# Performance work log

Hardware: AMD Instinct MI355X
Metric: run time of the kernel (lower is better)

The kernel has to match this reference:

```python
import jax, jax.numpy as jnp
import numpy as np

EPS_BN = 1e-5
EPS_NORM = 1e-12
USER_NUM, ITEM_NUM = 100000, 50000
N_NODES = USER_NUM + ITEM_NUM
N_EDGES = 2400000
OUT_DIM, HID_DIM = 64, 128
BATCH = 4096


def setup_inputs() -> dict:
    key = jax.random.key(0)
    ks = jax.random.split(key, 12)
    f32 = jnp.float32
    return {
        "user_emb": jax.random.normal(ks[0], (USER_NUM, OUT_DIM), f32) * 0.1,
        "item_emb": jax.random.normal(ks[1], (ITEM_NUM, OUT_DIM), f32) * 0.1,
        "W0": jax.random.normal(ks[2], (OUT_DIM, HID_DIM), f32) * (1.0 / np.sqrt(OUT_DIM)),
        "b0": jnp.zeros((HID_DIM,), f32),
        "g0": jnp.ones((HID_DIM,), f32),
        "beta0": jnp.zeros((HID_DIM,), f32),
        "W1": jax.random.normal(ks[3], (HID_DIM, HID_DIM), f32) * (1.0 / np.sqrt(HID_DIM)),
        "b1": jnp.zeros((HID_DIM,), f32),
        "g1": jnp.ones((HID_DIM,), f32),
        "beta1": jnp.zeros((HID_DIM,), f32),
        "W2": jax.random.normal(ks[4], (HID_DIM, OUT_DIM), f32) * (1.0 / np.sqrt(HID_DIM)),
        "b2": jnp.zeros((OUT_DIM,), f32),
        "user_id": jax.random.randint(ks[5], (BATCH,), 0, USER_NUM),
        "pos_item": jax.random.randint(ks[6], (BATCH,), 0, ITEM_NUM),
        "neg_item": jax.random.randint(ks[7], (BATCH,), 0, ITEM_NUM),
        "edge_index": jax.random.randint(ks[8], (2, N_EDGES), 0, N_NODES),
    }


def _gcn_conv(x, W, b, src, dst, dis):
    # GCNConv with self-loops and symmetric normalization:
    # out_i = sum_{j->i} d_j^{-1/2} d_i^{-1/2} (x_j W) + d_i^{-1} (x_i W) + b
    h = x @ W                                   # [N, F]
    norm = dis[src] * dis[dst]                  # [E]
    msgs = h[src] * norm[:, None]               # [E, F] (irregular gather)
    agg = jax.ops.segment_sum(msgs, dst, num_segments=x.shape[0])
    self_loop = h * (dis * dis)[:, None]        # contribution of added self-loops
    return agg + self_loop + b


def _bn_train(x, gamma, beta):
    mean = jnp.mean(x, axis=0)
    var = jnp.mean((x - mean) ** 2, axis=0)     # biased var, as torch BN uses
    return (x - mean) * jax.lax.rsqrt(var + EPS_BN) * gamma + beta


def _l2norm(x):
    n = jnp.sqrt(jnp.sum(x * x, axis=-1, keepdims=True))
    return x / jnp.maximum(n, EPS_NORM)


def reference(user_emb, item_emb, W0, b0, g0, beta0, W1, b1, g1, beta1, W2, b2,
              user_id, pos_item, neg_item, edge_index):
    N = user_emb.shape[0] + item_emb.shape[0]
    src, dst = edge_index[0], edge_index[1]
    # degree includes self loop (weight 1 per edge + 1 self loop)
    deg = 1.0 + jax.ops.segment_sum(jnp.ones_like(src, user_emb.dtype), dst, num_segments=N)
    dis = jax.lax.rsqrt(deg)

    x = jnp.concatenate([user_emb, item_emb], axis=0)          # [N, OUT_DIM]

    # layer 0: conv -> BN -> ReLU -> (dropout: eval/identity) -> L2-normalize
    x = _l2norm(jax.nn.relu(_bn_train(_gcn_conv(x, W0, b0, src, dst, dis), g0, beta0)))
    # layer 1
    x = _l2norm(jax.nn.relu(_bn_train(_gcn_conv(x, W1, b1, src, dst, dis), g1, beta1)))
    # final conv
    x = _gcn_conv(x, W2, b2, src, dst, dis)                    # [N, OUT_DIM]

    user_embeddings = x[:user_emb.shape[0]]
    item_embeddings = x[user_emb.shape[0]:]
    u = user_embeddings[user_id]
    p = item_embeddings[pos_item]
    n = item_embeddings[neg_item]
    pos_score = jnp.sum(u * p, axis=-1)
    neg_score = jnp.sum(u * n, axis=-1)
    rec_loss = -jnp.mean(jax.nn.log_sigmoid(pos_score - neg_score))
    return rec_loss, x
```

## Files before the change

kernel.cpp:

```cpp
#include <hip/hip_runtime.h>
#include <hip/hip_bf16.h>
#include <math.h>

#define USER_NUM 100000
#define ITEM_NUM 50000
#define N_NODES  150000
#define N_EDGES  2400000
#define OUT_DIM  64
#define HID_DIM  128
#define BATCH    4096
#define EPS_BN   1e-5f

typedef unsigned short ushort_t;
typedef unsigned int uint_t;

typedef __attribute__((ext_vector_type(8))) __bf16 bf16x8;
typedef __attribute__((ext_vector_type(4))) float f32x4;

__device__ __forceinline__ ushort_t f2bf(float f) {
    uint_t u = __float_as_uint(f);
    u += 0x7FFFu + ((u >> 16) & 1u);
    return (ushort_t)(u >> 16);
}
__device__ __forceinline__ float bf2f(ushort_t s) {
    return __uint_as_float((uint_t)s << 16);
}


__global__ __launch_bounds__(256) void zero_int_kernel(int* __restrict__ p, int n) {
    int i = blockIdx.x * 256 + threadIdx.x;
    if (i < n) p[i] = 0;
}

__global__ __launch_bounds__(256) void count_kernel(const int* __restrict__ dst, int* __restrict__ cnt) {
    int i = blockIdx.x * 256 + threadIdx.x;
    if (i < N_EDGES) atomicAdd(&cnt[dst[i]], 1);
}

__global__ __launch_bounds__(256) void dis_kernel(const int* __restrict__ cnt, float* __restrict__ dis) {
    int i = blockIdx.x * 256 + threadIdx.x;
    if (i < N_NODES) dis[i] = rsqrtf(1.0f + (float)cnt[i]);
}

#define SC_ELEM 1024
#define SC_NB   ((N_NODES + SC_ELEM - 1) / SC_ELEM)

__global__ __launch_bounds__(256) void scan_part_kernel(const int* __restrict__ cnt,
                                                        int* __restrict__ psum) {
    __shared__ int red[4];
    int tid = threadIdx.x;
    int base = blockIdx.x * SC_ELEM + tid * 4;
    int s = 0;
#pragma unroll
    for (int j = 0; j < 4; j++) { int i = base + j; if (i < N_NODES) s += cnt[i]; }
#pragma unroll
    for (int d = 1; d < 64; d <<= 1) s += __shfl_xor(s, d);
    if ((tid & 63) == 0) red[tid >> 6] = s;
    __syncthreads();
    if (tid == 0) psum[blockIdx.x] = red[0] + red[1] + red[2] + red[3];
}

__global__ __launch_bounds__(256) void scan_mid_kernel(int* __restrict__ psum,
                                                       int* __restrict__ off, int nb) {
    __shared__ int lds[256];
    int tid = threadIdx.x;
    int v = (tid < nb) ? psum[tid] : 0;
    lds[tid] = v;
    __syncthreads();
    for (int d = 1; d < 256; d <<= 1) {
        int t = (tid >= d) ? lds[tid - d] : 0;
        __syncthreads();
        lds[tid] += t;
        __syncthreads();
    }
    if (tid < nb) psum[tid] = lds[tid] - v;
    if (tid == 0) off[N_NODES] = lds[255];
}

__global__ __launch_bounds__(256) void scan_emit_kernel(const int* __restrict__ cnt,
                                                        const int* __restrict__ psum,
                                                        int* __restrict__ off) {
    __shared__ int lds[256];
    int tid = threadIdx.x;
    int base = blockIdx.x * SC_ELEM + tid * 4;
    int v[4]; int s = 0;
#pragma unroll
    for (int j = 0; j < 4; j++) {
        int i = base + j;
        v[j] = (i < N_NODES) ? cnt[i] : 0;
        s += v[j];
    }
    lds[tid] = s;
    __syncthreads();
    for (int d = 1; d < 256; d <<= 1) {
        int t = (tid >= d) ? lds[tid - d] : 0;
        __syncthreads();
        lds[tid] += t;
        __syncthreads();
    }
    int run = psum[blockIdx.x] + lds[tid] - s;
#pragma unroll
    for (int j = 0; j < 4; j++) {
        int i = base + j;
        if (i < N_NODES) off[i] = run;
        run += v[j];
    }
}


#define BSH   9
#define NBUCK ((N_NODES + 511) / 512)
#define P1_BLOCKS 512

__global__ __launch_bounds__(256) void bucket_part_kernel(const int* __restrict__ src,
                                                          const int* __restrict__ dst,
                                                          const int* __restrict__ off,
                                                          int* __restrict__ bcur,
                                                          uint2* __restrict__ temp) {
    __shared__ int hist[NBUCK];
    __shared__ int base[NBUCK];
    const int per = (N_EDGES + P1_BLOCKS - 1) / P1_BLOCKS;
    const int lo = blockIdx.x * per;
    int hi = lo + per; if (hi > N_EDGES) hi = N_EDGES;
    const int tid = threadIdx.x;
    for (int j = tid; j < NBUCK; j += 256) hist[j] = 0;
    __syncthreads();
    for (int i = lo + tid; i < hi; i += 256)
        atomicAdd(&hist[dst[i] >> BSH], 1);
    __syncthreads();
    for (int b = tid; b < NBUCK; b += 256) {
        int h = hist[b];
        if (h > 0) base[b] = off[b << BSH] + atomicAdd(&bcur[b], h);
    }
    __syncthreads();
    for (int i = lo + tid; i < hi; i += 256) {
        int d = dst[i];
        int p = atomicAdd(&base[d >> BSH], 1);
        temp[p] = make_uint2((uint_t)src[i], (uint_t)d);
    }
}

__global__ __launch_bounds__(256) void bucket_fine_kernel(const int* __restrict__ off,
                                                          const float* __restrict__ dis,
                                                          const uint2* __restrict__ temp,
                                                          uint2* __restrict__ csr8) {
    __shared__ int   offs[513];
    __shared__ int   cur[512];
    __shared__ float disd[512];
    const int b  = blockIdx.x;
    const int lo = b << BSH;
    int hi = lo + 512; if (hi > N_NODES) hi = N_NODES;
    const int nn = hi - lo;
    const int tid = threadIdx.x;
    for (int j = tid; j <= nn; j += 256) offs[j] = off[lo + j];
    for (int j = tid; j < nn; j += 256) { cur[j] = 0; disd[j] = dis[lo + j]; }
    __syncthreads();
    const int e0 = offs[0], e1 = offs[nn];
    for (int i = e0 + tid; i < e1; i += 256) {
        uint2 t = temp[i];
        int dl = (int)t.y - lo;
        int p = offs[dl] + atomicAdd(&cur[dl], 1);
        float wv = dis[t.x] * disd[dl];
        csr8[p] = make_uint2(t.x, __float_as_uint(wv));
    }
}


__device__ __forceinline__ bf16x8 loadA(const ushort_t* p) {
    uint4 u = *(const uint4*)p;
    return __builtin_bit_cast(bf16x8, u);
}
__device__ __forceinline__ bf16x8 loadA(const float* p) {
    float4 f0 = *(const float4*)p;
    float4 f1 = *(const float4*)(p + 4);
    uint4 u;
    u.x = (uint_t)f2bf(f0.x) | ((uint_t)f2bf(f0.y) << 16);
    u.y = (uint_t)f2bf(f0.z) | ((uint_t)f2bf(f0.w) << 16);
    u.z = (uint_t)f2bf(f1.x) | ((uint_t)f2bf(f1.y) << 16);
    u.w = (uint_t)f2bf(f1.z) | ((uint_t)f2bf(f1.w) << 16);
    return __builtin_bit_cast(bf16x8, u);
}

template<typename XT, int DIN, int DOUT>
__global__ __launch_bounds__(256) void gemm_kernel(const XT* __restrict__ xlo,
                                                   const XT* __restrict__ xhi, int split,
                                                   const float* __restrict__ W,
                                                   ushort_t* __restrict__ out, int nrows) {
    constexpr int LDW = DIN + 8;
    constexpr int NCT = DOUT / 16;
    __shared__ ushort_t wt[DOUT][LDW];

    const int tid = threadIdx.x;
    for (int idx = tid; idx < DIN * DOUT; idx += 256) {
        int k = idx / DOUT, n = idx % DOUT;
        wt[n][k] = f2bf(W[idx]);
    }
    __syncthreads();

    const int wave = tid >> 6, lane = tid & 63;
    const int lm = lane & 15, lk = lane >> 4;
    const int row0 = blockIdx.x * 128 + wave * 32;

    f32x4 acc[2][NCT];
#pragma unroll
    for (int rt = 0; rt < 2; rt++)
#pragma unroll
        for (int c = 0; c < NCT; c++) acc[rt][c] = (f32x4){0.f, 0.f, 0.f, 0.f};

    const XT* rp[2];
#pragma unroll
    for (int rt = 0; rt < 2; rt++) {
        int row = row0 + rt * 16 + lm;
        if (row > nrows - 1) row = nrows - 1;
        rp[rt] = (row < split) ? xlo + (size_t)row * DIN
                               : xhi + (size_t)(row - split) * DIN;
    }

#pragma unroll
    for (int ks = 0; ks < DIN / 32; ks++) {
        bf16x8 a0 = loadA(rp[0] + ks * 32 + lk * 8);
        bf16x8 a1 = loadA(rp[1] + ks * 32 + lk * 8);
#pragma unroll
        for (int c = 0; c < NCT; c++) {
            bf16x8 b = *(const bf16x8*)&wt[c * 16 + lm][ks * 32 + lk * 8];
            acc[0][c] = __builtin_amdgcn_mfma_f32_16x16x32_bf16(a0, b, acc[0][c], 0, 0, 0);
            acc[1][c] = __builtin_amdgcn_mfma_f32_16x16x32_bf16(a1, b, acc[1][c], 0, 0, 0);
        }
    }

#pragma unroll
    for (int rt = 0; rt < 2; rt++) {
#pragma unroll
        for (int r = 0; r < 4; r++) {
            int row = row0 + rt * 16 + lk * 4 + r;
            if (row < nrows) {
#pragma unroll
                for (int c = 0; c < NCT; c++)
                    out[(size_t)row * DOUT + c * 16 + lm] = f2bf(acc[rt][c][r]);
            }
        }
    }
}


template<int DOUT>
__global__ __launch_bounds__(256) void agg_kernel(const ushort_t* __restrict__ h,
                                                  const float* __restrict__ dis,
                                                  const int* __restrict__ off,
                                                  const uint2* __restrict__ csr8,
                                                  const float* __restrict__ bias,
                                                  float* __restrict__ out, int n) {
    int wave = threadIdx.x >> 6;
    int lane = threadIdx.x & 63;
    int node = blockIdx.x * 4 + wave;
    if (node >= n) return;
    float di  = dis[node];
    int   beg = off[node], end = off[node + 1];
    if (DOUT == 128) {
        const uint_t* hp = (const uint_t*)h;
        float ax = 0.f, ay = 0.f;
        int e = beg;
        for (; e + 4 <= end; e += 4) {
            uint2 e0 = csr8[e], e1 = csr8[e + 1], e2 = csr8[e + 2], e3 = csr8[e + 3];
            uint_t u0 = hp[(size_t)e0.x * 64 + lane];
            uint_t u1 = hp[(size_t)e1.x * 64 + lane];
            uint_t u2 = hp[(size_t)e2.x * 64 + lane];
            uint_t u3 = hp[(size_t)e3.x * 64 + lane];
            float w0 = __uint_as_float(e0.y), w1 = __uint_as_float(e1.y);
            float w2 = __uint_as_float(e2.y), w3 = __uint_as_float(e3.y);
            ax = fmaf(__uint_as_float(u0 << 16), w0, ax);
            ay = fmaf(__uint_as_float(u0 & 0xFFFF0000u), w0, ay);
            ax = fmaf(__uint_as_float(u1 << 16), w1, ax);
            ay = fmaf(__uint_as_float(u1 & 0xFFFF0000u), w1, ay);
            ax = fmaf(__uint_as_float(u2 << 16), w2, ax);
            ay = fmaf(__uint_as_float(u2 & 0xFFFF0000u), w2, ay);
            ax = fmaf(__uint_as_float(u3 << 16), w3, ax);
            ay = fmaf(__uint_as_float(u3 & 0xFFFF0000u), w3, ay);
        }
        for (; e < end; e++) {
            uint2 ev = csr8[e];
            float wv = __uint_as_float(ev.y);
            uint_t u = hp[(size_t)ev.x * 64 + lane];
            ax = fmaf(__uint_as_float(u << 16), wv, ax);
            ay = fmaf(__uint_as_float(u & 0xFFFF0000u), wv, ay);
        }
        uint_t us = hp[(size_t)node * 64 + lane];
        float2 bb = ((const float2*)bias)[lane];
        float dd = di * di;
        float2 o;
        o.x = ax + __uint_as_float(us << 16) * dd + bb.x;
        o.y = ay + __uint_as_float(us & 0xFFFF0000u) * dd + bb.y;
        ((float2*)out)[(size_t)node * 64 + lane] = o;
    } else {
        float ax = 0.f;
        int e = beg;
        for (; e + 4 <= end; e += 4) {
            uint2 e0 = csr8[e], e1 = csr8[e + 1], e2 = csr8[e + 2], e3 = csr8[e + 3];
            float h0 = bf2f(h[(size_t)e0.x * 64 + lane]);
            float h1 = bf2f(h[(size_t)e1.x * 64 + lane]);
            float h2 = bf2f(h[(size_t)e2.x * 64 + lane]);
            float h3 = bf2f(h[(size_t)e3.x * 64 + lane]);
            ax = fmaf(h0, __uint_as_float(e0.y), ax);
            ax = fmaf(h1, __uint_as_float(e1.y), ax);
            ax = fmaf(h2, __uint_as_float(e2.y), ax);
            ax = fmaf(h3, __uint_as_float(e3.y), ax);
        }
        for (; e < end; e++) {
            uint2 ev = csr8[e];
            ax = fmaf(bf2f(h[(size_t)ev.x * 64 + lane]), __uint_as_float(ev.y), ax);
        }
        float hs = bf2f(h[(size_t)node * 64 + lane]);
        out[(size_t)node * 64 + lane] = ax + hs * di * di + bias[lane];
    }
}


#define STATS_NB 512

__global__ __launch_bounds__(128) void stats1_kernel(const float* __restrict__ x,
                                                     double* __restrict__ part) {
    int col = threadIdx.x;
    double a = 0.0, b = 0.0;
    for (int row = blockIdx.x; row < N_NODES; row += STATS_NB) {
        float v = x[(size_t)row * HID_DIM + col];
        a += v;
        b += (double)v * (double)v;
    }
    part[(size_t)blockIdx.x * 256 + col]       = a;
    part[(size_t)blockIdx.x * 256 + 128 + col] = b;
}

__global__ __launch_bounds__(256) void stats2_kernel(const double* __restrict__ part,
                                                     const float* __restrict__ g,
                                                     const float* __restrict__ beta,
                                                     float* __restrict__ a_out,
                                                     float* __restrict__ b_out) {
    __shared__ double red1[4], red2[4];
    int col = blockIdx.x;
    int tid = threadIdx.x;
    double s1 = 0.0, s2 = 0.0;
    for (int p = tid; p < STATS_NB; p += 256) {
        s1 += part[(size_t)p * 256 + col];
        s2 += part[(size_t)p * 256 + 128 + col];
    }
#pragma unroll
    for (int d = 32; d >= 1; d >>= 1) {
        s1 += __shfl_xor(s1, d);
        s2 += __shfl_xor(s2, d);
    }
    int wave = tid >> 6, lane = tid & 63;
    if (lane == 0) { red1[wave] = s1; red2[wave] = s2; }
    __syncthreads();
    if (tid == 0) {
        double t1 = red1[0] + red1[1] + red1[2] + red1[3];
        double t2 = red2[0] + red2[1] + red2[2] + red2[3];
        double mean = t1 / (double)N_NODES;
        double var  = t2 / (double)N_NODES - mean * mean;
        float inv = rsqrtf((float)var + EPS_BN);
        float aa  = g[col] * inv;
        a_out[col] = aa;
        b_out[col] = beta[col] - (float)mean * aa;
    }
}


__global__ __launch_bounds__(256) void bn_relu_l2_kernel(const float* __restrict__ in,
                                                         const float* __restrict__ a,
                                                         const float* __restrict__ b,
                                                         uint_t* __restrict__ outp, int n) {
    int wave = threadIdx.x >> 6;
    int lane = threadIdx.x & 63;
    int row  = blockIdx.x * 4 + wave;
    if (row >= n) return;
    float2 v  = *(const float2*)(in + (size_t)row * 128 + lane * 2);
    float2 aa = *(const float2*)(a + lane * 2);
    float2 bb = *(const float2*)(b + lane * 2);
    float y0 = fmaxf(fmaf(v.x, aa.x, bb.x), 0.f);
    float y1 = fmaxf(fmaf(v.y, aa.y, bb.y), 0.f);
    float ss = y0 * y0 + y1 * y1;
#pragma unroll
    for (int d = 32; d >= 1; d >>= 1) ss += __shfl_xor(ss, d);
    float nn  = sqrtf(ss);
    float inv = 1.f / fmaxf(nn, 1e-12f);
    uint_t pk = (uint_t)f2bf(y0 * inv) | ((uint_t)f2bf(y1 * inv) << 16);
    outp[(size_t)row * 64 + lane] = pk;
}


__global__ void zero_float_kernel(float* p) { *p = 0.f; }

__global__ __launch_bounds__(256) void loss_kernel(const float* __restrict__ X,
                                                   const int* __restrict__ uid,
                                                   const int* __restrict__ pid,
                                                   const int* __restrict__ nid,
                                                   float* __restrict__ out0) {
    int wave = threadIdx.x >> 6;
    int lane = threadIdx.x & 63;
    int b = blockIdx.x * 4 + wave;
    if (b >= BATCH) return;
    const float* u = X + (size_t)uid[b] * OUT_DIM;
    const float* p = X + (size_t)(USER_NUM + pid[b]) * OUT_DIM;
    const float* q = X + (size_t)(USER_NUM + nid[b]) * OUT_DIM;
    float uv = u[lane];
    float ps = uv * p[lane];
    float ns = uv * q[lane];
#pragma unroll
    for (int d = 32; d >= 1; d >>= 1) {
        ps += __shfl_xor(ps, d);
        ns += __shfl_xor(ns, d);
    }
    if (lane == 0) {
        float t  = ns - ps;
        float sp = fmaxf(t, 0.f) + log1pf(expf(-fabsf(t)));
        atomicAdd(out0, sp * (1.0f / BATCH));
    }
}


extern "C" void kernel_launch(void* const* d_in, const int* in_sizes, int n_in,
                              void* d_out, int out_size, void* d_ws, size_t ws_size,
                              hipStream_t stream) {
    const float* user_emb = (const float*)d_in[0];
    const float* item_emb = (const float*)d_in[1];
    const float* W0  = (const float*)d_in[2];
    const float* b0  = (const float*)d_in[3];
    const float* g0  = (const float*)d_in[4];
    const float* be0 = (const float*)d_in[5];
    const float* W1  = (const float*)d_in[6];
    const float* b1  = (const float*)d_in[7];
    const float* g1  = (const float*)d_in[8];
    const float* be1 = (const float*)d_in[9];
    const float* W2  = (const float*)d_in[10];
    const float* b2  = (const float*)d_in[11];
    const int* user_id  = (const int*)d_in[12];
    const int* pos_item = (const int*)d_in[13];
    const int* neg_item = (const int*)d_in[14];
    const int* edge     = (const int*)d_in[15];
    const int* src = edge;
    const int* dst = edge + N_EDGES;

    char* w = (char*)d_ws;
    auto alloc = [&](size_t bytes) -> char* {
        char* r = w;
        w += (bytes + 255) / 256 * 256;
        return r;
    };
    int*      cnt  = (int*)alloc((size_t)N_NODES * 4);
    int*      off  = (int*)alloc((size_t)(N_NODES + 1) * 4);
    int*      bcur = (int*)alloc((size_t)NBUCK * 4);
    uint2*    csr8 = (uint2*)alloc((size_t)N_EDGES * 8);
    float*    dis  = (float*)alloc((size_t)N_NODES * 4);
    int*      psum = (int*)alloc((size_t)SC_NB * 4);
    double*   part = (double*)alloc((size_t)STATS_NB * 256 * 8);
    float*    bn_a = (float*)alloc(128 * 4);
    float*    bn_b = (float*)alloc(128 * 4);
    ushort_t* hbuf = (ushort_t*)alloc((size_t)N_NODES * HID_DIM * 2);
    float*    xbuf = (float*)alloc((size_t)N_NODES * HID_DIM * 4);
    ushort_t* xbf  = (ushort_t*)alloc((size_t)N_NODES * HID_DIM * 2);

    uint2* temp = (uint2*)hbuf;

    float* out = (float*)d_out;
    float* X   = out + 1;

    const int EB = (N_EDGES + 255) / 256;
    const int NB = (N_NODES + 255) / 256;
    const int AGGB = (N_NODES + 3) / 4;
    const int GB = (N_NODES + 127) / 128;

    zero_int_kernel<<<NB, 256, 0, stream>>>(cnt, N_NODES);
    count_kernel<<<EB, 256, 0, stream>>>(dst, cnt);
    dis_kernel<<<NB, 256, 0, stream>>>(cnt, dis);
    scan_part_kernel<<<SC_NB, 256, 0, stream>>>(cnt, psum);
    scan_mid_kernel<<<1, 256, 0, stream>>>(psum, off, SC_NB);
    scan_emit_kernel<<<SC_NB, 256, 0, stream>>>(cnt, psum, off);
    zero_int_kernel<<<(NBUCK + 255) / 256, 256, 0, stream>>>(bcur, NBUCK);
    bucket_part_kernel<<<P1_BLOCKS, 256, 0, stream>>>(src, dst, off, bcur, temp);
    bucket_fine_kernel<<<NBUCK, 256, 0, stream>>>(off, dis, temp, csr8);

    gemm_kernel<float, 64, 128><<<GB, 256, 0, stream>>>(
        user_emb, item_emb, USER_NUM, W0, hbuf, N_NODES);
    agg_kernel<128><<<AGGB, 256, 0, stream>>>(hbuf, dis, off, csr8, b0, xbuf, N_NODES);
    stats1_kernel<<<STATS_NB, 128, 0, stream>>>(xbuf, part);
    stats2_kernel<<<128, 256, 0, stream>>>(part, g0, be0, bn_a, bn_b);
    bn_relu_l2_kernel<<<AGGB, 256, 0, stream>>>(xbuf, bn_a, bn_b, (uint_t*)xbf, N_NODES);

    gemm_kernel<ushort_t, 128, 128><<<GB, 256, 0, stream>>>(
        xbf, xbf, N_NODES, W1, hbuf, N_NODES);
    agg_kernel<128><<<AGGB, 256, 0, stream>>>(hbuf, dis, off, csr8, b1, xbuf, N_NODES);
    stats1_kernel<<<STATS_NB, 128, 0, stream>>>(xbuf, part);
    stats2_kernel<<<128, 256, 0, stream>>>(part, g1, be1, bn_a, bn_b);
    bn_relu_l2_kernel<<<AGGB, 256, 0, stream>>>(xbuf, bn_a, bn_b, (uint_t*)xbf, N_NODES);

    gemm_kernel<ushort_t, 128, 64><<<GB, 256, 0, stream>>>(
        xbf, xbf, N_NODES, W2, hbuf, N_NODES);
    agg_kernel<64><<<AGGB, 256, 0, stream>>>(hbuf, dis, off, csr8, b2, X, N_NODES);

    zero_float_kernel<<<1, 1, 0, stream>>>(out);
    loss_kernel<<<(BATCH + 3) / 4, 256, 0, stream>>>(X, user_id, pos_item, neg_item, out);
}
```

Before: 967.5 us.

## Fuse BN statistics into persistent aggregation kernel with deeper gather unroll

Result: no change. 955.1 us (-1.3%).

```diff
diff --git a/kernel.cpp b/kernel.cpp
--- a/kernel.cpp
+++ b/kernel.cpp
@@ -13,6 +13,7 @@
 
 typedef unsigned short ushort_t;
 typedef unsigned int uint_t;
+typedef unsigned long long ull_t;
 
 typedef __attribute__((ext_vector_type(8))) __bf16 bf16x8;
 typedef __attribute__((ext_vector_type(4))) float f32x4;
@@ -236,101 +237,111 @@
             if (row < nrows) {
 #pragma unroll
                 for (int c = 0; c < NCT; c++)
-                    out[(size_t)row * DOUT + c * 16 + lm] = f2bf(acc[rt][c][r]);
+                    __builtin_nontemporal_store(f2bf(acc[rt][c][r]),
+                                                &out[(size_t)row * DOUT + c * 16 + lm]);
             }
         }
     }
 }
 
 
-template<int DOUT>
+#define AGG_BLOCKS 2048
+#define NPART (AGG_BLOCKS * 4)
+
+template<int DOUT, bool STATS>
 __global__ __launch_bounds__(256) void agg_kernel(const ushort_t* __restrict__ h,
                                                   const float* __restrict__ dis,
                                                   const int* __restrict__ off,
                                                   const uint2* __restrict__ csr8,
                                                   const float* __restrict__ bias,
-                                                  float* __restrict__ out, int n) {
-    int wave = threadIdx.x >> 6;
-    int lane = threadIdx.x & 63;
-    int node = blockIdx.x * 4 + wave;
-    if (node >= n) return;
-    float di  = dis[node];
-    int   beg = off[node], end = off[node + 1];
-    if (DOUT == 128) {
-        const uint_t* hp = (const uint_t*)h;
-        float ax = 0.f, ay = 0.f;
-        int e = beg;
-        for (; e + 4 <= end; e += 4) {
-            uint2 e0 = csr8[e], e1 = csr8[e + 1], e2 = csr8[e + 2], e3 = csr8[e + 3];
-            uint_t u0 = hp[(size_t)e0.x * 64 + lane];
-            uint_t u1 = hp[(size_t)e1.x * 64 + lane];
-            uint_t u2 = hp[(size_t)e2.x * 64 + lane];
-            uint_t u3 = hp[(size_t)e3.x * 64 + lane];
-            float w0 = __uint_as_float(e0.y), w1 = __uint_as_float(e1.y);
-            float w2 = __uint_as_float(e2.y), w3 = __uint_as_float(e3.y);
-            ax = fmaf(__uint_as_float(u0 << 16), w0, ax);
-            ay = fmaf(__uint_as_float(u0 & 0xFFFF0000u), w0, ay);
-            ax = fmaf(__uint_as_float(u1 << 16), w1, ax);
-            ay = fmaf(__uint_as_float(u1 & 0xFFFF0000u), w1, ay);
-            ax = fmaf(__uint_as_float(u2 << 16), w2, ax);
-            ay = fmaf(__uint_as_float(u2 & 0xFFFF0000u), w2, ay);
-            ax = fmaf(__uint_as_float(u3 << 16), w3, ax);
-            ay = fmaf(__uint_as_float(u3 & 0xFFFF0000u), w3, ay);
+                                                  float* __restrict__ out,
+                                                  float* __restrict__ part, int n) {
+    const int wave = threadIdx.x >> 6;
+    const int lane = threadIdx.x & 63;
+    const int gw   = blockIdx.x * 4 + wave;
+    const int NW   = AGG_BLOCKS * 4;
+
+    float s1x = 0.f, s2x = 0.f, s1y = 0.f, s2y = 0.f;
+
+    for (int node = gw; node < n; node += NW) {
+        float di  = dis[node];
+        int   beg = off[node], end = off[node + 1];
+        if (DOUT == 128) {
+            const uint_t* hp = (const uint_t*)h;
+            float ax = 0.f, ay = 0.f;
+            int e = beg;
+            for (; e + 8 <= end; e += 8) {
+                ull_t c[8];
+#pragma unroll
+                for (int j = 0; j < 8; j++)
+                    c[j] = __builtin_nontemporal_load((const ull_t*)&csr8[e + j]);
+                uint_t u[8];
+#pragma unroll
+                for (int j = 0; j < 8; j++)
+                    u[j] = hp[(size_t)(uint_t)c[j] * 64 + lane];
+#pragma unroll
+                for (int j = 0; j < 8; j++) {
+                    float wv = __uint_as_float((uint_t)(c[j] >> 32));
+                    ax = fmaf(__uint_as_float(u[j] << 16), wv, ax);
+                    ay = fmaf(__uint_as_float(u[j] & 0xFFFF0000u), wv, ay);
+                }
+            }
+            for (; e < end; e++) {
+                ull_t cv = __builtin_nontemporal_load((const ull_t*)&csr8[e]);
+                float wv = __uint_as_float((uint_t)(cv >> 32));
+                uint_t u = hp[(size_t)(uint_t)cv * 64 + lane];
+                ax = fmaf(__uint_as_float(u << 16), wv, ax);
+                ay = fmaf(__uint_as_float(u & 0xFFFF0000u), wv, ay);
+            }
+            uint_t us = hp[(size_t)node * 64 + lane];
+            float2 bb = ((const float2*)bias)[lane];
+            float dd = di * di;
+            float ox = ax + __uint_as_float(us << 16) * dd + bb.x;
+            float oy = ay + __uint_as_float(us & 0xFFFF0000u) * dd + bb.y;
+            ull_t obits = __builtin_bit_cast(ull_t, make_float2(ox, oy));
+            __builtin_nontemporal_store(obits, (ull_t*)&((float2*)out)[(size_t)node * 64 + lane]);
+            if (STATS) {
+                s1x += ox; s2x = fmaf(ox, ox, s2x);
+                s1y += oy; s2y = fmaf(oy, oy, s2y);
+            }
+        } else {
+            float ax = 0.f;
+            int e = beg;
+            for (; e + 8 <= end; e += 8) {
+                ull_t c[8];
+#pragma unroll
+                for (int j = 0; j < 8; j++)
+                    c[j] = __builtin_nontemporal_load((const ull_t*)&csr8[e + j]);
+                float hv[8];
+#pragma unroll
+                for (int j = 0; j < 8; j++)
+                    hv[j] = bf2f(h[(size_t)(uint_t)c[j] * 64 + lane]);
+#pragma unroll
+                for (int j = 0; j < 8; j++)
+                    ax = fmaf(hv[j], __uint_as_float((uint_t)(c[j] >> 32)), ax);
+            }
+            for (; e < end; e++) {
+                ull_t cv = __builtin_nontemporal_load((const ull_t*)&csr8[e]);
+                ax = fmaf(bf2f(h[(size_t)(uint_t)cv * 64 + lane]),
+                          __uint_as_float((uint_t)(cv >> 32)), ax);
+            }
+            float hs = bf2f(h[(size_t)node * 64 + lane]);
+            float ox = ax + hs * di * di + bias[lane];
+            __builtin_nontemporal_store(ox, &out[(size_t)node * 64 + lane]);
         }
-        for (; e < end; e++) {
-            uint2 ev = csr8[e];
-            float wv = __uint_as_float(ev.y);
-            uint_t u = hp[(size_t)ev.x * 64 + lane];
-            ax = fmaf(__uint_as_float(u << 16), wv, ax);
-            ay = fmaf(__uint_as_float(u & 0xFFFF0000u), wv, ay);
-        }
-        uint_t us = hp[(size_t)node * 64 + lane];
-        float2 bb = ((const float2*)bias)[lane];
-        float dd = di * di;
-        float2 o;
-        o.x = ax + __uint_as_float(us << 16) * dd + bb.x;
-        o.y = ay + __uint_as_float(us & 0xFFFF0000u) * dd + bb.y;
-        ((float2*)out)[(size_t)node * 64 + lane] = o;
-    } else {
-        float ax = 0.f;
-        int e = beg;
-        for (; e + 4 <= end; e += 4) {
-            uint2 e0 = csr8[e], e1 = csr8[e + 1], e2 = csr8[e + 2], e3 = csr8[e + 3];
-            float h0 = bf2f(h[(size_t)e0.x * 64 + lane]);
-            float h1 = bf2f(h[(size_t)e1.x * 64 + lane]);
-            float h2 = bf2f(h[(size_t)e2.x * 64 + lane]);
-            float h3 = bf2f(h[(size_t)e3.x * 64 + lane]);
-            ax = fmaf(h0, __uint_as_float(e0.y), ax);
-            ax = fmaf(h1, __uint_as_float(e1.y), ax);
-            ax = fmaf(h2, __uint_as_float(e2.y), ax);
-            ax = fmaf(h3, __uint_as_float(e3.y), ax);
-        }
-        for (; e < end; e++) {
-            uint2 ev = csr8[e];
-            ax = fmaf(bf2f(h[(size_t)ev.x * 64 + lane]), __uint_as_float(ev.y), ax);
-        }
-        float hs = bf2f(h[(size_t)node * 64 + lane]);
-        out[(size_t)node * 64 + lane] = ax + hs * di * di + bias[lane];
-    }
-}
-
-
-#define STATS_NB 512
-
-__global__ __launch_bounds__(128) void stats1_kernel(const float* __restrict__ x,
-                                                     double* __restrict__ part) {
-    int col = threadIdx.x;
-    double a = 0.0, b = 0.0;
-    for (int row = blockIdx.x; row < N_NODES; row += STATS_NB) {
-        float v = x[(size_t)row * HID_DIM + col];
-        a += v;
-        b += (double)v * (double)v;
-    }
-    part[(size_t)blockIdx.x * 256 + col]       = a;
-    part[(size_t)blockIdx.x * 256 + 128 + col] = b;
-}
-
-__global__ __launch_bounds__(256) void stats2_kernel(const double* __restrict__ part,
+    }
+
+    if (STATS) {
+        float* pp = part + (size_t)gw * 256;
+        pp[lane * 2]           = s1x;
+        pp[lane * 2 + 1]       = s1y;
+        pp[128 + lane * 2]     = s2x;
+        pp[128 + lane * 2 + 1] = s2y;
+    }
+}
+
+
+__global__ __launch_bounds__(256) void stats2_kernel(const float* __restrict__ part,
                                                      const float* __restrict__ g,
                                                      const float* __restrict__ beta,
                                                      float* __restrict__ a_out,
@@ -339,9 +350,9 @@
     int col = blockIdx.x;
     int tid = threadIdx.x;
     double s1 = 0.0, s2 = 0.0;
-    for (int p = tid; p < STATS_NB; p += 256) {
-        s1 += part[(size_t)p * 256 + col];
-        s2 += part[(size_t)p * 256 + 128 + col];
+    for (int p = tid; p < NPART; p += 256) {
+        s1 += (double)part[(size_t)p * 256 + col];
+        s2 += (double)part[(size_t)p * 256 + 128 + col];
     }
 #pragma unroll
     for (int d = 32; d >= 1; d >>= 1) {
@@ -451,7 +462,7 @@
     uint2*    csr8 = (uint2*)alloc((size_t)N_EDGES * 8);
     float*    dis  = (float*)alloc((size_t)N_NODES * 4);
     int*      psum = (int*)alloc((size_t)SC_NB * 4);
-    double*   part = (double*)alloc((size_t)STATS_NB * 256 * 8);
+    float*    part = (float*)alloc((size_t)NPART * 256 * 4);
     float*    bn_a = (float*)alloc(128 * 4);
     float*    bn_b = (float*)alloc(128 * 4);
     ushort_t* hbuf = (ushort_t*)alloc((size_t)N_NODES * HID_DIM * 2);
@@ -465,7 +476,7 @@
 
     const int EB = (N_EDGES + 255) / 256;
     const int NB = (N_NODES + 255) / 256;
-    const int AGGB = (N_NODES + 3) / 4;
+    const int BNB = (N_NODES + 3) / 4;
     const int GB = (N_NODES + 127) / 128;
 
     zero_int_kernel<<<NB, 256, 0, stream>>>(cnt, N_NODES);
@@ -480,21 +491,22 @@
 
     gemm_kernel<float, 64, 128><<<GB, 256, 0, stream>>>(
         user_emb, item_emb, USER_NUM, W0, hbuf, N_NODES);
-    agg_kernel<128><<<AGGB, 256, 0, stream>>>(hbuf, dis, off, csr8, b0, xbuf, N_NODES);
-    stats1_kernel<<<STATS_NB, 128, 0, stream>>>(xbuf, part);
+    agg_kernel<128, true><<<AGG_BLOCKS, 256, 0, stream>>>(
+        hbuf, dis, off, csr8, b0, xbuf, part, N_NODES);
     stats2_kernel<<<128, 256, 0, stream>>>(part, g0, be0, bn_a, bn_b);
-    bn_relu_l2_kernel<<<AGGB, 256, 0, stream>>>(xbuf, bn_a, bn_b, (uint_t*)xbf, N_NODES);
+    bn_relu_l2_kernel<<<BNB, 256, 0, stream>>>(xbuf, bn_a, bn_b, (uint_t*)xbf, N_NODES);
 
     gemm_kernel<ushort_t, 128, 128><<<GB, 256, 0, stream>>>(
         xbf, xbf, N_NODES, W1, hbuf, N_NODES);
-    agg_kernel<128><<<AGGB, 256, 0, stream>>>(hbuf, dis, off, csr8, b1, xbuf, N_NODES);
-    stats1_kernel<<<STATS_NB, 128, 0, stream>>>(xbuf, part);
+    agg_kernel<128, true><<<AGG_BLOCKS, 256, 0, stream>>>(
+        hbuf, dis, off, csr8, b1, xbuf, part, N_NODES);
     stats2_kernel<<<128, 256, 0, stream>>>(part, g1, be1, bn_a, bn_b);
-    bn_relu_l2_kernel<<<AGGB, 256, 0, stream>>>(xbuf, bn_a, bn_b, (uint_t*)xbf, N_NODES);
+    bn_relu_l2_kernel<<<BNB, 256, 0, stream>>>(xbuf, bn_a, bn_b, (uint_t*)xbf, N_NODES);
 
     gemm_kernel<ushort_t, 128, 64><<<GB, 256, 0, stream>>>(
         xbf, xbf, N_NODES, W2, hbuf, N_NODES);
-    agg_kernel<64><<<AGGB, 256, 0, stream>>>(hbuf, dis, off, csr8, b2, X, N_NODES);
+    agg_kernel<64, false><<<AGG_BLOCKS, 256, 0, stream>>>(
+        hbuf, dis, off, csr8, b2, X, part, N_NODES);
 
     zero_float_kernel<<<1, 1, 0, stream>>>(out);
     loss_kernel<<<(BATCH + 3) / 4, 256, 0, stream>>>(X, user_id, pos_item, neg_item, out);
```
